# Kernel optimization log

Hardware: AMD Instinct MI355X
Metric: run time of the kernel (lower is better)

Reference implementation:

```python
import jax, jax.numpy as jnp
import numpy as np

POOL = 7  # pool_size = (7, 7)


def setup_inputs() -> dict:
    key = jax.random.key(0)
    k1, k2, k3 = jax.random.split(key, 3)
    B, H, W, C = 1, 128, 128, 512
    N = 1024
    feature_maps = jax.random.normal(k1, (B, H, W, C), dtype=jnp.float32)
    # rois = (x1, y1, x2, y2) int coords, guaranteed x2 > x1, y2 > y1 (min size 8)
    xy1 = jax.random.randint(k2, (N, 2), 0, W - 8)
    wh = jax.random.randint(k3, (N, 2), 8, 64)
    x2 = jnp.minimum(xy1[:, 0] + wh[:, 0], W)
    y2 = jnp.minimum(xy1[:, 1] + wh[:, 1], H)
    rois = jnp.stack([xy1[:, 0], xy1[:, 1], x2, y2], axis=1).astype(jnp.int32)
    return {"feature_maps": feature_maps, "rois": rois}


def _half_pixel_coords(start, size, out_size):
    # tf.image.resize (TF2 bilinear) uses half-pixel centers:
    #   src = (dst + 0.5) * (in / out) - 0.5, clamped to [0, in-1]
    sizef = size.astype(jnp.float32)
    scale = sizef / out_size
    c = (jnp.arange(out_size, dtype=jnp.float32) + 0.5) * scale - 0.5
    c = jnp.clip(c, 0.0, sizef - 1.0)
    return c + start.astype(jnp.float32)


def reference(feature_maps, rois):
    # feature_maps: [B, H, W, C]; rois: [N, 4] int (x1, y1, x2, y2)
    def pool_one(roi):
        x1, y1, x2, y2 = roi[0], roi[1], roi[2], roi[3]
        ys = _half_pixel_coords(y1, y2 - y1, POOL)  # [7] absolute y coords
        xs = _half_pixel_coords(x1, x2 - x1, POOL)  # [7] absolute x coords
        y0 = jnp.floor(ys).astype(jnp.int32)
        x0 = jnp.floor(xs).astype(jnp.int32)
        y1i = jnp.minimum(y0 + 1, y2 - 1)  # clamp within crop (edge replicate)
        x1i = jnp.minimum(x0 + 1, x2 - 1)
        wy = (ys - y0.astype(jnp.float32))[None, :, None, None]
        wx = (xs - x0.astype(jnp.float32))[None, None, :, None]
        tl = feature_maps[:, y0[:, None], x0[None, :], :]   # [B,7,7,C]
        tr = feature_maps[:, y0[:, None], x1i[None, :], :]
        bl = feature_maps[:, y1i[:, None], x0[None, :], :]
        br = feature_maps[:, y1i[:, None], x1i[None, :], :]
        top = tl + (tr - tl) * wx
        bot = bl + (br - bl) * wx
        return top + (bot - top) * wy  # [B, 7, 7, C]

    # tf.map_fn over rois stacks per-roi results -> [N, B, 7, 7, C]
    return jax.vmap(pool_one)(rois)
```

## Files before the change

kernel.cpp:

```cpp
#include <hip/hip_runtime.h>


#define POOLN 7
#define FM_W 128
#define FM_C 512
#define NXCD 8
#define CHUNK_C 64
#define BINS_PER_ITER 16
#define NGROUPS 256
#define STRIDE (BINS_PER_ITER * NGROUPS)

typedef float f32x4 __attribute__((ext_vector_type(4)));

__global__ __launch_bounds__(256) void roi_align_kernel(
    const float* __restrict__ fm,
    const int* __restrict__ rois,
    float* __restrict__ out,
    int n_bins)
{
    const int chunk = blockIdx.x & (NXCD - 1);
    const int group = blockIdx.x >> 3;
    const int lane  = threadIdx.x & 15;
    const int sub   = threadIdx.x >> 4;
    const int coff  = chunk * CHUNK_C + lane * 4;

    auto coords = [&](int b, int& oa, int& ob, int& od, int& oe,
                      float& wxo, float& wyo) {
        const int roi = b / 49;
        const int rem = b - roi * 49;
        const int py  = rem / 7;
        const int px  = rem - py * 7;

        const int4 r = reinterpret_cast<const int4*>(rois)[roi];
        const int x1 = r.x, y1 = r.y, x2 = r.z, y2 = r.w;

        const float sizy = (float)(y2 - y1);
        float cy = ((float)py + 0.5f) * (sizy / (float)POOLN) - 0.5f;
        cy = fminf(fmaxf(cy, 0.0f), sizy - 1.0f);
        const float ys = cy + (float)y1;
        const int   y0 = (int)floorf(ys);
        const int   yb = min(y0 + 1, y2 - 1);
        wyo = ys - (float)y0;

        const float sizx = (float)(x2 - x1);
        float cx = ((float)px + 0.5f) * (sizx / (float)POOLN) - 0.5f;
        cx = fminf(fmaxf(cx, 0.0f), sizx - 1.0f);
        const float xs = cx + (float)x1;
        const int   x0 = (int)floorf(xs);
        const int   xb = min(x0 + 1, x2 - 1);
        wxo = xs - (float)x0;

        oa = (y0 * FM_W + x0) * FM_C + coff;
        ob = (y0 * FM_W + xb) * FM_C + coff;
        od = (yb * FM_W + x0) * FM_C + coff;
        oe = (yb * FM_W + xb) * FM_C + coff;
    };

    int bin = group * BINS_PER_ITER + sub;
    int oa, ob, od, oe;
    float wx, wy;
    coords(bin, oa, ob, od, oe, wx, wy);
    f32x4 a  = *reinterpret_cast<const f32x4*>(fm + oa);
    f32x4 bb = *reinterpret_cast<const f32x4*>(fm + ob);
    f32x4 d  = *reinterpret_cast<const f32x4*>(fm + od);
    f32x4 e  = *reinterpret_cast<const f32x4*>(fm + oe);

    for (;;) {
        const int nbin = bin + STRIDE;
        const bool nv = nbin < n_bins;

        f32x4 na, nb, nd, ne;
        float nwx = 0.f, nwy = 0.f;
        if (nv) {
            int qa, qb, qd, qe;
            coords(nbin, qa, qb, qd, qe, nwx, nwy);
            na = *reinterpret_cast<const f32x4*>(fm + qa);
            nb = *reinterpret_cast<const f32x4*>(fm + qb);
            nd = *reinterpret_cast<const f32x4*>(fm + qd);
            ne = *reinterpret_cast<const f32x4*>(fm + qe);
        }

        const f32x4 top = a + (bb - a) * wx;
        const f32x4 bot = d + (e - d) * wx;
        const f32x4 res = top + (bot - top) * wy;
        f32x4* o = reinterpret_cast<f32x4*>(out + (size_t)bin * FM_C + coff);
        __builtin_nontemporal_store(res, o);

        if (!nv) break;
        bin = nbin; wx = nwx; wy = nwy;
        a = na; bb = nb; d = nd; e = ne;
    }
}

extern "C" void kernel_launch(void* const* d_in, const int* in_sizes, int n_in,
                              void* d_out, int out_size, void* d_ws, size_t ws_size,
                              hipStream_t stream) {
    const float* fm   = (const float*)d_in[0];
    const int*   rois = (const int*)d_in[1];
    float*       out  = (float*)d_out;

    const int N      = in_sizes[1] / 4;
    const int n_bins = N * POOLN * POOLN;
    dim3 grid(NGROUPS * NXCD);
    roi_align_kernel<<<grid, 256, 0, stream>>>(fm, rois, out, n_bins);
}
```

Measured before the change: 32.35 us.

## Assign one block per ROI and split bins across channel-wide sub-warps

Replaces the grid-stride bin scheme, where each XCD handled one 64-channel slice, with one 512-thread block per ROI. Four sub-groups of 128 lanes each cover all 512 channels and stride over the 49 bins. ROI coordinates are loaded once per block, and ROIs are mapped to XCDs in contiguous ranges so that overlapping ROI reads may share L2. The trade-off is that the per-XCD channel partitioning of the feature map is gone, so each XCD's L2 may now see the whole feature map rather than one slice.

```diff
diff --git a/kernel.cpp b/kernel.cpp
--- a/kernel.cpp
+++ b/kernel.cpp
@@ -5,36 +5,37 @@
 #define FM_W 128
 #define FM_C 512
 #define NXCD 8
-#define CHUNK_C 64
-#define BINS_PER_ITER 16
-#define NGROUPS 256
-#define STRIDE (BINS_PER_ITER * NGROUPS)
 
 typedef float f32x4 __attribute__((ext_vector_type(4)));
 
-__global__ __launch_bounds__(256) void roi_align_kernel(
+__global__ __launch_bounds__(512) void roi_align_kernel(
     const float* __restrict__ fm,
     const int* __restrict__ rois,
     float* __restrict__ out,
-    int n_bins)
+    int nroi)
 {
-    const int chunk = blockIdx.x & (NXCD - 1);
-    const int group = blockIdx.x >> 3;
-    const int lane  = threadIdx.x & 15;
-    const int sub   = threadIdx.x >> 4;
-    const int coff  = chunk * CHUNK_C + lane * 4;
+    int roi;
+    if ((nroi & (NXCD - 1)) == 0) {
+        const int per = nroi >> 3;
+        roi = (blockIdx.x & (NXCD - 1)) * per + (blockIdx.x >> 3);
+    } else {
+        roi = blockIdx.x;
+    }
 
-    auto coords = [&](int b, int& oa, int& ob, int& od, int& oe,
+    const int sub  = threadIdx.x >> 7;
+    const int lane = threadIdx.x & 127;
+    const int coff = lane * 4;
+
+    const int4 r = reinterpret_cast<const int4*>(rois)[roi];
+    const int x1 = r.x, y1 = r.y, x2 = r.z, y2 = r.w;
+    const float sizx = (float)(x2 - x1);
+    const float sizy = (float)(y2 - y1);
+
+    auto coords = [&](int bl, int& oa, int& ob, int& od, int& oe,
                       float& wxo, float& wyo) {
-        const int roi = b / 49;
-        const int rem = b - roi * 49;
-        const int py  = rem / 7;
-        const int px  = rem - py * 7;
+        const int py = bl / 7;
+        const int px = bl - py * 7;
 
-        const int4 r = reinterpret_cast<const int4*>(rois)[roi];
-        const int x1 = r.x, y1 = r.y, x2 = r.z, y2 = r.w;
-
-        const float sizy = (float)(y2 - y1);
         float cy = ((float)py + 0.5f) * (sizy / (float)POOLN) - 0.5f;
         cy = fminf(fmaxf(cy, 0.0f), sizy - 1.0f);
         const float ys = cy + (float)y1;
@@ -42,7 +43,6 @@
         const int   yb = min(y0 + 1, y2 - 1);
         wyo = ys - (float)y0;
 
-        const float sizx = (float)(x2 - x1);
         float cx = ((float)px + 0.5f) * (sizx / (float)POOLN) - 0.5f;
         cx = fminf(fmaxf(cx, 0.0f), sizx - 1.0f);
         const float xs = cx + (float)x1;
@@ -56,24 +56,26 @@
         oe = (yb * FM_W + xb) * FM_C + coff;
     };
 
-    int bin = group * BINS_PER_ITER + sub;
+    int bl = sub;
     int oa, ob, od, oe;
     float wx, wy;
-    coords(bin, oa, ob, od, oe, wx, wy);
+    coords(bl, oa, ob, od, oe, wx, wy);
     f32x4 a  = *reinterpret_cast<const f32x4*>(fm + oa);
     f32x4 bb = *reinterpret_cast<const f32x4*>(fm + ob);
     f32x4 d  = *reinterpret_cast<const f32x4*>(fm + od);
     f32x4 e  = *reinterpret_cast<const f32x4*>(fm + oe);
 
+    const size_t obase = (size_t)roi * 49 * FM_C + coff;
+
     for (;;) {
-        const int nbin = bin + STRIDE;
-        const bool nv = nbin < n_bins;
+        const int  nbl = bl + 4;
+        const bool nv  = nbl < 49;
 
         f32x4 na, nb, nd, ne;
         float nwx = 0.f, nwy = 0.f;
         if (nv) {
             int qa, qb, qd, qe;
-            coords(nbin, qa, qb, qd, qe, nwx, nwy);
+            coords(nbl, qa, qb, qd, qe, nwx, nwy);
             na = *reinterpret_cast<const f32x4*>(fm + qa);
             nb = *reinterpret_cast<const f32x4*>(fm + qb);
             nd = *reinterpret_cast<const f32x4*>(fm + qd);
@@ -83,11 +85,11 @@
         const f32x4 top = a + (bb - a) * wx;
         const f32x4 bot = d + (e - d) * wx;
         const f32x4 res = top + (bot - top) * wy;
-        f32x4* o = reinterpret_cast<f32x4*>(out + (size_t)bin * FM_C + coff);
+        f32x4* o = reinterpret_cast<f32x4*>(out + obase + (size_t)bl * FM_C);
         __builtin_nontemporal_store(res, o);
 
         if (!nv) break;
-        bin = nbin; wx = nwx; wy = nwy;
+        bl = nbl; wx = nwx; wy = nwy;
         a = na; bb = nb; d = nd; e = ne;
     }
 }
@@ -99,8 +101,6 @@
     const int*   rois = (const int*)d_in[1];
     float*       out  = (float*)d_out;
 
-    const int N      = in_sizes[1] / 4;
-    const int n_bins = N * POOLN * POOLN;
-    dim3 grid(NGROUPS * NXCD);
-    roi_align_kernel<<<grid, 256, 0, stream>>>(fm, rois, out, n_bins);
+    const int N = in_sizes[1] / 4;
+    roi_align_kernel<<<N, 512, 0, stream>>>(fm, rois, out, N);
 }
```

New measurement: 65.74 us. 2.03x slower.
